# Kernel tuning notes

Measured on AMD Instinct MI355X. Metric: run time of the kernel, lower is better.

Reference implementation:

```python
import jax, jax.numpy as jnp
import numpy as np

KNN = 5
MAX_STEPS = 100
LAM = 1.0  # bound_lambda


def setup_inputs() -> dict:
    key = jax.random.key(0)
    k1, k2 = jax.random.split(key)
    # probabilities in (0,1): softmax-like scores
    scores_raw = jax.random.uniform(k1, (1, 8192, 8, 8), dtype=jnp.float32)
    feats = jax.random.normal(k2, (1, 8192, 256, 1, 1), dtype=jnp.float32)
    return {"scores_raw": scores_raw, "feats": feats}


def knn_affinity(X, knn):
    # X: (N, D) L2-normalized features. Same math as torch.norm(x_i - x_j):
    # ||xi-xj|| = sqrt(|xi|^2 + |xj|^2 - 2 xi.xj), avoids the O(N^2 D) broadcast.
    N = X.shape[0]
    sq = jnp.sum(X * X, axis=-1)                                  # (N,)
    dist2 = sq[:, None] + sq[None, :] - 2.0 * (X @ X.T)           # (N, N)
    dist = jnp.sqrt(jnp.maximum(dist2, 0.0))
    n_neighbors = min(knn + 1, N)
    _, idx = jax.lax.top_k(-dist, n_neighbors)                    # smallest distances
    idx = idx[:, 1:]                                              # drop self
    W = jnp.zeros((N, N), X.dtype).at[jnp.arange(N)[:, None], idx].set(1.0)
    return W


def reference(scores_raw, feats):
    _, _, H, W = scores_raw.shape
    unary = -jnp.log(scores_raw.reshape(-1, H * W) + 1e-10)       # (N, K)
    f = feats.reshape(feats.shape[0], feats.shape[1], -1)[0]       # (N, D), flatten(-3).squeeze(0)
    nrm = jnp.linalg.norm(f, axis=-1, keepdims=True)
    f = f / jnp.maximum(nrm, 1e-12)                                # F.normalize(p=2)
    kernel = knn_affinity(f, KNN)                                  # (N, N)

    Y0 = jax.nn.softmax(-unary, axis=-1)

    def cond(state):
        i, Y, oldE, conv = state
        return (i < MAX_STEPS) & (~conv)

    def body(state):
        i, Y, oldE, _ = state
        pairwise = LAM * (kernel @ Y)                              # (N, K)
        Ynew = jax.nn.softmax(-unary + pairwise, axis=-1)
        # entropy_energy (note: lambda multiplies pairwise again, as in source)
        E = jnp.sum(unary * Ynew - LAM * pairwise * Ynew
                    + Ynew * jnp.log(jnp.clip(Ynew, 1e-20)))
        conv = (i > 1) & (jnp.abs(E - oldE) <= 1e-8 * jnp.abs(oldE))
        return (i + 1, Ynew, E, conv)

    init = (jnp.int32(0), Y0, jnp.float32(jnp.inf), jnp.bool_(False))
    _, Y, _, _ = jax.lax.while_loop(cond, body, init)
    return Y
```

## Files before the change

kernel.cpp:

```cpp
#include <hip/hip_runtime.h>
#include <math.h>

#define NROWS 8192
#define DIM   256
#define NCLS  64
#define KNN   5
#define NCAND 8
#define NSPLIT 4
#define MAXSTEPS 100
#define PBLK 256

struct GS {
  double Eold;
  double Epart[PBLK];
  int pad0[30];
  int gcnt[16 * 32];
  int root; int pad1[31];
  int gen;  int pad2[31];
  int flag; int pad3[31];
};

typedef __attribute__((ext_vector_type(8))) short bf16x8;
typedef __attribute__((ext_vector_type(4))) float f32x4;

typedef __attribute__((address_space(1))) unsigned int glb_u32_t;
typedef __attribute__((address_space(3))) unsigned int lds_u32_t;
__device__ __forceinline__ void async_cp16(const uint4* g, uint4* l) {
  __builtin_amdgcn_global_load_lds((const glb_u32_t*)(const unsigned int*)g,
                                   (lds_u32_t*)(unsigned int*)l, 16, 0, 0);
}

__device__ __forceinline__ float aloadf(const float* p) {
  return __hip_atomic_load(p, __ATOMIC_RELAXED, __HIP_MEMORY_SCOPE_AGENT);
}
__device__ __forceinline__ void astoref(float* p, float v) {
  __hip_atomic_store(p, v, __ATOMIC_RELAXED, __HIP_MEMORY_SCOPE_AGENT);
}
__device__ __forceinline__ double aloadd(const double* p) {
  return __hip_atomic_load(p, __ATOMIC_RELAXED, __HIP_MEMORY_SCOPE_AGENT);
}
__device__ __forceinline__ void astored(double* p, double v) {
  __hip_atomic_store(p, v, __ATOMIC_RELAXED, __HIP_MEMORY_SCOPE_AGENT);
}
__device__ __forceinline__ int aloadi(const int* p) {
  return __hip_atomic_load(p, __ATOMIC_RELAXED, __HIP_MEMORY_SCOPE_AGENT);
}
__device__ __forceinline__ void astorei(int* p, int v) {
  __hip_atomic_store(p, v, __ATOMIC_RELAXED, __HIP_MEMORY_SCOPE_AGENT);
}
__device__ __forceinline__ int afetchadd(int* p) {
  return __hip_atomic_fetch_add(p, 1, __ATOMIC_RELAXED, __HIP_MEMORY_SCOPE_AGENT);
}

__device__ __forceinline__ float wave_sum64(float v) {
#pragma unroll
  for (int m = 32; m >= 1; m >>= 1) v += __shfl_xor(v, m, 64);
  return v;
}
__device__ __forceinline__ double wave_sum64d(double v) {
#pragma unroll
  for (int m = 32; m >= 1; m >>= 1) v += __shfl_xor(v, m, 64);
  return v;
}

__device__ __forceinline__ unsigned short f2bf(float x) {
  unsigned u = __float_as_uint(x);
  u += 0x7FFFu + ((u >> 16) & 1u);
  return (unsigned short)(u >> 16);
}

__device__ __forceinline__ void cs_desc(unsigned& a, unsigned& b) {
  unsigned hi = a > b ? a : b;
  unsigned lo = a > b ? b : a;
  a = hi; b = lo;
}

__global__ void k_normalize(const float* __restrict__ feats, uint2* __restrict__ fb2,
                            float* __restrict__ f, double* __restrict__ sqd,
                            GS* __restrict__ gs) {
  if (blockIdx.x == 0) {
    int tt = threadIdx.x;
    if (tt == 0) {
      gs->Eold = (double)INFINITY;
      gs->root = 0; gs->gen = 0; gs->flag = 0;
    }
    if (tt < 256) { gs->gcnt[tt] = 0; gs->gcnt[tt + 256] = 0; }
  }
  int row  = blockIdx.x * 4 + (threadIdx.x >> 6);
  int lane = threadIdx.x & 63;
  float4 v = ((const float4*)(feats + (size_t)row * DIM))[lane];
  double ss = (double)v.x * v.x + (double)v.y * v.y + (double)v.z * v.z + (double)v.w * v.w;
  ss = wave_sum64d(ss);
  float nr = fmaxf((float)sqrt(ss), 1e-12f);
  float4 o;
  o.x = v.x / nr; o.y = v.y / nr; o.z = v.z / nr; o.w = v.w / nr;
  ((float4*)(f + (size_t)row * DIM))[lane] = o;
  double s2 = (double)o.x * o.x + (double)o.y * o.y + (double)o.z * o.z + (double)o.w * o.w;
  s2 = wave_sum64d(s2);
  if (lane == 0) sqd[row] = s2;
  uint2 w2;
  w2.x = (unsigned)f2bf(o.x) | ((unsigned)f2bf(o.y) << 16);
  w2.y = (unsigned)f2bf(o.z) | ((unsigned)f2bf(o.w) << 16);
  int T = row >> 6, rl = row & 63, g = lane >> 1, h = lane & 1;
  fb2[((size_t)T * 2048 + rl * 32 + (g ^ (rl & 31))) * 2 + h] = w2;
}

#define JSPAN (NROWS / NSPLIT)
#define GTILES (JSPAN / 64)

__launch_bounds__(512, 4)
__global__ void k_gram(const uint4* __restrict__ fb, int* __restrict__ candp) {
  __shared__ uint4 Bsh4[2][2048];

  const int t  = threadIdx.x;
  const int L  = (blockIdx.x & 7) * 64 + (blockIdx.x >> 3);
  const int js = L >> 7;
  const int ib = L & 127;
  const int i0 = ib * 64;
  const int jbase = js * JSPAN;
  const int w = t >> 6, lane = t & 63;
  const int ap = w >> 2;
  const int sb = w & 3;
  const int m15 = lane & 15, quad = lane >> 4;

  {
    const uint4* At = fb + (size_t)ib * 2048;
    const uint4* Bt = fb + (size_t)(js * 32) * 2048;
#pragma unroll
    for (int p = 0; p < 4; ++p) {
      int c = w * 4 + p;
      async_cp16(At + c * 64 + lane, &Bsh4[1][c * 64]);
      async_cp16(Bt + c * 64 + lane, &Bsh4[0][c * 64]);
    }
  }
  __syncthreads();

  bf16x8 areg[2][8];
#pragma unroll
  for (int st = 0; st < 2; ++st) {
    int ra = ap * 32 + st * 16 + m15;
#pragma unroll
    for (int kc = 0; kc < 8; ++kc)
      areg[st][kc] = ((const bf16x8*)Bsh4[1])[ra * 32 + ((kc * 4 + quad) ^ (ra & 31))];
  }
  __syncthreads();

  unsigned mk[2][NCAND];
#pragma unroll
  for (int st = 0; st < 2; ++st)
#pragma unroll
    for (int k = 0; k < NCAND; ++k) mk[st][k] = 0u;
  float thr[2] = {-1e30f, -1e30f};

  const int rb = sb * 16 + m15;

  for (int jt = 0; jt < GTILES; ++jt) {
    const int cbuf = jt & 1;
    if (jt > 0) __syncthreads();
    if (jt + 1 < GTILES) {
      const uint4* Bt = fb + (size_t)(js * 32 + jt + 1) * 2048;
#pragma unroll
      for (int p = 0; p < 4; ++p) {
        int c = w * 4 + p;
        async_cp16(Bt + c * 64 + lane, &Bsh4[1 - cbuf][c * 64]);
      }
    }

    f32x4 acc[2];
    acc[0] = (f32x4)(0.f); acc[1] = (f32x4)(0.f);
#pragma unroll
    for (int kc = 0; kc < 8; ++kc) {
      bf16x8 bv = ((const bf16x8*)Bsh4[cbuf])[rb * 32 + ((kc * 4 + quad) ^ (rb & 31))];
      acc[0] = __builtin_amdgcn_mfma_f32_16x16x32_bf16(bv, areg[0][kc], acc[0], 0, 0, 0);
      acc[1] = __builtin_amdgcn_mfma_f32_16x16x32_bf16(bv, areg[1][kc], acc[1], 0, 0, 0);
    }

    const unsigned cbase = (unsigned)(jt * 64 + sb * 16 + quad * 4);
#pragma unroll
    for (int st = 0; st < 2; ++st) {
      f32x4 v = acc[st];
      float g4 = fmaxf(fmaxf(v[0], v[1]), fmaxf(v[2], v[3]));
      if (g4 > thr[st]) {
        unsigned n[4];
#pragma unroll
        for (int e = 0; e < 4; ++e) {
          unsigned ub = __float_as_uint(v[e]);
          n[e] = ((ub ^ (unsigned)(((int)ub >> 31) | 0x80000000)) & ~2047u)
                 | (cbase + (unsigned)e);
        }
        cs_desc(n[0], n[1]); cs_desc(n[2], n[3]);
        cs_desc(n[0], n[2]); cs_desc(n[1], n[3]);
        cs_desc(n[1], n[2]);
        unsigned m[8];
        m[0] = mk[st][0]; m[1] = mk[st][1]; m[2] = mk[st][2]; m[3] = mk[st][3];
        m[4] = mk[st][4] > n[3] ? mk[st][4] : n[3];
        m[5] = mk[st][5] > n[2] ? mk[st][5] : n[2];
        m[6] = mk[st][6] > n[1] ? mk[st][6] : n[1];
        m[7] = mk[st][7] > n[0] ? mk[st][7] : n[0];
        cs_desc(m[0], m[4]); cs_desc(m[1], m[5]); cs_desc(m[2], m[6]); cs_desc(m[3], m[7]);
        cs_desc(m[0], m[2]); cs_desc(m[1], m[3]); cs_desc(m[4], m[6]); cs_desc(m[5], m[7]);
        cs_desc(m[0], m[1]); cs_desc(m[2], m[3]); cs_desc(m[4], m[5]); cs_desc(m[6], m[7]);
#pragma unroll
        for (int i = 0; i < 8; ++i) mk[st][i] = m[i];
        unsigned kb = mk[st][NCAND - 1] & ~2047u;
        if (kb) {
          unsigned xm = 0x80000000u | ~(unsigned)((int)kb >> 31);
          thr[st] = __uint_as_float(kb ^ xm);
        }
      }
    }
  }

  __syncthreads();
  unsigned* Ksh = (unsigned*)Bsh4;
#pragma unroll
  for (int st = 0; st < 2; ++st) {
    int row = ap * 32 + st * 16 + m15;
    int slot0 = (sb * 4 + quad) * 8;
#pragma unroll
    for (int k = 0; k < NCAND; ++k)
      Ksh[row * 128 + ((slot0 + k + row) & 127)] = mk[st][k];
  }
  __syncthreads();
  if (t < 64) {
    unsigned fk[NCAND];
#pragma unroll
    for (int k = 0; k < NCAND; ++k) fk[k] = 0u;
    for (int ss = 0; ss < 128; ++ss) {
      unsigned kk = Ksh[t * 128 + ((ss + t) & 127)];
      if (kk > fk[NCAND - 1]) {
        fk[NCAND - 1] = kk;
#pragma unroll
        for (int q = NCAND - 1; q >= 1; --q)
          if (fk[q] > fk[q - 1]) { unsigned tm = fk[q]; fk[q] = fk[q - 1]; fk[q - 1] = tm; }
      }
    }
#pragma unroll
    for (int k = 0; k < NCAND; ++k)
      candp[(size_t)js * (NROWS * NCAND) + (size_t)(i0 + t) * NCAND + k] =
          jbase + (int)(fk[k] & 2047u);
  }
}

__global__ void k_refine(const float* __restrict__ f, const double* __restrict__ sqd,
                         const int* __restrict__ candp, int* __restrict__ nbr) {
  const int row = blockIdx.x * 4 + (threadIdx.x >> 6);
  const int t = threadIdx.x & 63;
  const int c = t >> 1;
  const int seg = t & 1;
  const int split = c >> 3, slot = c & 7;
  int j = candp[(size_t)split * (NROWS * NCAND) + (size_t)row * NCAND + slot];
  const float4* fi4 = (const float4*)(f + (size_t)row * DIM) + seg * 32;
  const float4* fj4 = (const float4*)(f + (size_t)j * DIM) + seg * 32;
  double dot = 0.0;
#pragma unroll 8
  for (int d4 = 0; d4 < 32; ++d4) {
    float4 a = fi4[d4], b = fj4[d4];
    dot = fma((double)a.x, (double)b.x, dot);
    dot = fma((double)a.y, (double)b.y, dot);
    dot = fma((double)a.z, (double)b.z, dot);
    dot = fma((double)a.w, (double)b.w, dot);
  }
  dot += __shfl_xor(dot, 1, 64);
  double key = sqd[j] - 2.0 * dot;
  bool valid = (seg == 0) && (j != row);
  for (int s = 0; s < KNN; ++s) {
    double v = valid ? key : (double)INFINITY;
    int vj = valid ? j : 0x7fffffff;
#pragma unroll
    for (int m = 1; m < 64; m <<= 1) {
      double ov = __shfl_xor(v, m, 64);
      int oj = __shfl_xor(vj, m, 64);
      if (ov < v || (ov == v && oj < vj)) { v = ov; vj = oj; }
    }
    if (valid && vj == j) valid = false;
    if (t == 0) nbr[(size_t)row * 8 + s] = vj;
  }
}

__launch_bounds__(1024, 4)
__global__ void k_solve(const float* __restrict__ scores,
                        const int* __restrict__ nbr,
                        float* __restrict__ Ya, float* __restrict__ Yb,
                        float* __restrict__ out, GS* __restrict__ gs) {
  const int b = blockIdx.x;
  const int w = threadIdx.x >> 6, lane = threadIdx.x & 63;
  const int row0 = b * 32 + w * 2;
  const int grp = (b & 15) * 32;
  __shared__ int nbl[32][5];
  __shared__ double sE[16];
  __shared__ int sflag;

  if (threadIdx.x < 160)
    nbl[threadIdx.x / 5][threadIdx.x % 5] =
        nbr[(size_t)(b * 32 + threadIdx.x / 5) * 8 + (threadIdx.x % 5)];

  float u[2], y[2];
#pragma unroll
  for (int r = 0; r < 2; ++r)
    u[r] = -logf(scores[(size_t)(row0 + r) * NCLS + lane] + 1e-10f);
#pragma unroll
  for (int r = 0; r < 2; ++r) {
    float e = expf(-u[r]);
    float sum = wave_sum64(e);
    y[r] = e / sum;
    astoref(&Ya[(size_t)(row0 + r) * NCLS + lane], y[r]);
  }
  __syncthreads();

  int nboff[2][KNN];
#pragma unroll
  for (int r = 0; r < 2; ++r)
#pragma unroll
    for (int k = 0; k < KNN; ++k)
      nboff[r][k] = nbl[w * 2 + r][k] * NCLS + lane;

  int mygen = 1;
  if (threadIdx.x == 0) {
    __builtin_amdgcn_fence(__ATOMIC_RELEASE, "workgroup");
    int old = afetchadd(&gs->gcnt[grp]);
    if (old == 15) {
      int r = afetchadd(&gs->root);
      if (r == 15) {
#pragma unroll
        for (int m = 0; m < 16; ++m) astorei(&gs->gcnt[m * 32], 0);
        astorei(&gs->root, 0);
        __builtin_amdgcn_fence(__ATOMIC_RELEASE, "workgroup");
        astorei(&gs->gen, mygen);
      }
    }
    while (aloadi(&gs->gen) < mygen) __builtin_amdgcn_s_sleep(1);
  }
  __syncthreads();
  ++mygen;

  for (int iter = 0; iter < MAXSTEPS; ++iter) {
    const float* __restrict__ Yin = (iter & 1) ? Yb : Ya;
    float* __restrict__ Yout = (iter & 1) ? Ya : Yb;
    double ew = 0.0;
#pragma unroll
    for (int r = 0; r < 2; ++r) {
      float pw = 0.f;
#pragma unroll
      for (int k = 0; k < KNN; ++k) pw += aloadf(&Yin[nboff[r][k]]);
      float e = expf(pw - u[r]);
      float sum = wave_sum64(e);
      y[r] = e / sum;
      astoref(&Yout[(size_t)(row0 + r) * NCLS + lane], y[r]);
      ew += -(double)logf(sum);
    }
    if (lane == 0) sE[w] = ew;
    __syncthreads();
    if (w == 0) {
      double be = (lane < 16) ? sE[lane] : 0.0;
      be = wave_sum64d(be);
      int last = 0;
      if (lane == 0) {
        astored(&gs->Epart[b], be);
        __builtin_amdgcn_fence(__ATOMIC_RELEASE, "workgroup");
        int old = afetchadd(&gs->gcnt[grp]);
        if (old == 15) {
          int r = afetchadd(&gs->root);
          last = (r == 15);
        }
      }
      last = __shfl(last, 0, 64);
      if (last) {
        double s = 0.0;
#pragma unroll
        for (int i = 0; i < 4; ++i) s += aloadd(&gs->Epart[lane + 64 * i]);
        s = wave_sum64d(s);
        if (lane < 16) astorei(&gs->gcnt[lane * 32], 0);
        if (lane == 0) {
          astorei(&gs->root, 0);
          double eo = aloadd(&gs->Eold);
          int conv = (iter > 1) && (fabs(s - eo) <= 1e-8 * fabs(eo));
          astorei(&gs->flag, conv);
          if (!conv) astored(&gs->Eold, s);
        }
        __builtin_amdgcn_fence(__ATOMIC_RELEASE, "workgroup");
        if (lane == 0) astorei(&gs->gen, mygen);
      }
      if (lane == 0) {
        while (aloadi(&gs->gen) < mygen) __builtin_amdgcn_s_sleep(1);
        sflag = aloadi(&gs->flag);
      }
    }
    __syncthreads();
    ++mygen;
    if (sflag) break;
  }

#pragma unroll
  for (int r = 0; r < 2; ++r)
    out[(size_t)(row0 + r) * NCLS + lane] = y[r];
}

extern "C" void kernel_launch(void* const* d_in, const int* in_sizes, int n_in,
                              void* d_out, int out_size, void* d_ws, size_t ws_size,
                              hipStream_t stream) {
  (void)in_sizes; (void)n_in; (void)out_size; (void)ws_size;
  const float* scores = (const float*)d_in[0];
  const float* feats  = (const float*)d_in[1];
  float* out = (float*)d_out;
  char* ws = (char*)d_ws;
  uint4*  fb    = (uint4*)(ws + 0);
  float*  f     = (float*)(ws + 4194304);
  float*  Ya    = (float*)(ws + 4194304);
  float*  Yb    = (float*)(ws + 6291456);
  double* sqd   = (double*)(ws + 12582912);
  int*    candp = (int*)(ws + 12648448);
  int*    nbr   = (int*)(ws + 13697024);
  GS*     gs    = (GS*)(ws + 13959168);

  k_normalize<<<NROWS / 4, 256, 0, stream>>>(feats, (uint2*)fb, f, sqd, gs);
  k_gram<<<(NROWS / 64) * NSPLIT, 512, 0, stream>>>(fb, candp);
  k_refine<<<NROWS / 4, 256, 0, stream>>>(f, sqd, candp, nbr);
  k_solve<<<PBLK, 1024, 0, stream>>>(scores, nbr, Ya, Yb, out, gs);
}
```

Measured before the change: 221.9 us.

## Defer energy convergence check off the grid barrier critical path

Moves the global energy reduction and convergence test out of the last-arriving block's barrier release path. Block 0 now reduces the previous iteration's double-buffered partials while waiting, and publishes a convN flag that is folded into the root atomic counter. This shortens the serialized work per grid barrier, but convergence is detected one iteration later, which may change the output if convergence occurs.

```diff
diff --git a/kernel.cpp b/kernel.cpp
--- a/kernel.cpp
+++ b/kernel.cpp
@@ -12,12 +12,13 @@
 
 struct GS {
   double Eold;
-  double Epart[PBLK];
+  double Epart[2][PBLK];
   int pad0[30];
   int gcnt[16 * 32];
   int root; int pad1[31];
   int gen;  int pad2[31];
   int flag; int pad3[31];
+  int convN; int pad4[31];
 };
 
 typedef __attribute__((ext_vector_type(8))) short bf16x8;
@@ -50,6 +51,9 @@
 }
 __device__ __forceinline__ int afetchadd(int* p) {
   return __hip_atomic_fetch_add(p, 1, __ATOMIC_RELAXED, __HIP_MEMORY_SCOPE_AGENT);
+}
+__device__ __forceinline__ int afetchaddv(int* p, int v) {
+  return __hip_atomic_fetch_add(p, v, __ATOMIC_RELAXED, __HIP_MEMORY_SCOPE_AGENT);
 }
 
 __device__ __forceinline__ float wave_sum64(float v) {
@@ -82,7 +86,7 @@
     int tt = threadIdx.x;
     if (tt == 0) {
       gs->Eold = (double)INFINITY;
-      gs->root = 0; gs->gen = 0; gs->flag = 0;
+      gs->root = 0; gs->gen = 0; gs->flag = 0; gs->convN = 0;
     }
     if (tt < 256) { gs->gcnt[tt] = 0; gs->gcnt[tt + 256] = 0; }
   }
@@ -334,6 +338,8 @@
   __syncthreads();
   ++mygen;
 
+  double Eold = (double)INFINITY;
+
   for (int iter = 0; iter < MAXSTEPS; ++iter) {
     const float* __restrict__ Yin = (iter & 1) ? Yb : Ya;
     float* __restrict__ Yout = (iter & 1) ? Ya : Yb;
@@ -354,32 +360,39 @@
     if (w == 0) {
       double be = (lane < 16) ? sE[lane] : 0.0;
       be = wave_sum64d(be);
-      int last = 0;
+      int last = 0, fl = 0;
       if (lane == 0) {
-        astored(&gs->Epart[b], be);
+        astored(&gs->Epart[iter & 1][b], be);
         __builtin_amdgcn_fence(__ATOMIC_RELEASE, "workgroup");
+        int cN = aloadi(&gs->convN);
         int old = afetchadd(&gs->gcnt[grp]);
         if (old == 15) {
-          int r = afetchadd(&gs->root);
-          last = (r == 15);
+          int r = afetchaddv(&gs->root, 1 + (cN << 8));
+          last = ((r & 255) == 15);
+          fl = ((r >> 8) + cN) != 0;
         }
       }
       last = __shfl(last, 0, 64);
       if (last) {
-        double s = 0.0;
-#pragma unroll
-        for (int i = 0; i < 4; ++i) s += aloadd(&gs->Epart[lane + 64 * i]);
-        s = wave_sum64d(s);
         if (lane < 16) astorei(&gs->gcnt[lane * 32], 0);
         if (lane == 0) {
           astorei(&gs->root, 0);
-          double eo = aloadd(&gs->Eold);
-          int conv = (iter > 1) && (fabs(s - eo) <= 1e-8 * fabs(eo));
-          astorei(&gs->flag, conv);
-          if (!conv) astored(&gs->Eold, s);
+          astorei(&gs->flag, fl);
+          __builtin_amdgcn_fence(__ATOMIC_RELEASE, "workgroup");
+          astorei(&gs->gen, mygen);
         }
-        __builtin_amdgcn_fence(__ATOMIC_RELEASE, "workgroup");
-        if (lane == 0) astorei(&gs->gen, mygen);
+      }
+      if (b == 0 && iter >= 1) {
+        const double* ep = gs->Epart[(iter + 1) & 1];
+        double s = 0.0;
+#pragma unroll
+        for (int i2 = 0; i2 < 4; ++i2) s += aloadd(&ep[lane + 64 * i2]);
+        s = wave_sum64d(s);
+        if (lane == 0) {
+          int cv = ((iter - 1) > 1) && (fabs(s - Eold) <= 1e-8 * fabs(Eold));
+          astorei(&gs->convN, cv);
+          if (!cv) Eold = s;
+        }
       }
       if (lane == 0) {
         while (aloadi(&gs->gen) < mygen) __builtin_amdgcn_s_sleep(1);
```

Result: slower. 227.4 us (+2.5%).
